# Optimization experiments

Measured on AMD Instinct MI355X. Metric: run time of the kernel, lower is better.

## Reference

```python
import jax, jax.numpy as jnp
import numpy as np

D_MODEL = 1024
N_HEAD = 16
B, S = 4, 1024


def setup_inputs() -> dict:
    key = jax.random.key(0)
    ks = jax.random.split(key, 10)
    f = lambda k, shp: jax.random.normal(k, shp, dtype=jnp.float32)
    return {
        "x": f(ks[0], (B, S, D_MODEL)),
        "y": f(ks[1], (B, S, D_MODEL)),
        "z": f(ks[2], (B, S, D_MODEL)),
        "mask": f(ks[3], (1, 1, S, S)) * 0.1,
        "wq_w": f(ks[4], (D_MODEL, D_MODEL)) * (D_MODEL ** -0.5),
        "wq_b": f(ks[5], (D_MODEL,)) * 0.02,
        "wk_w": f(ks[6], (D_MODEL, D_MODEL)) * (D_MODEL ** -0.5),
        "wk_b": f(ks[7], (D_MODEL,)) * 0.02,
        "wv_w": f(ks[8], (D_MODEL, D_MODEL)) * (D_MODEL ** -0.5),
        "wv_b": f(ks[9], (D_MODEL,)) * 0.02,
    }


def reference(x, y, z, mask, wq_w, wq_b, wk_w, wk_b, wv_w, wv_b):
    b, xl, d = x.shape
    hd = d // N_HEAD
    # linear projections (torch Linear: x @ W^T + b)
    q = x @ wq_w.T + wq_b
    k = y @ wk_w.T + wk_b
    v = z @ wv_w.T + wv_b
    # [B, H, L, hd]
    q = q.reshape(b, xl, N_HEAD, hd).transpose(0, 2, 1, 3)
    k = k.reshape(b, y.shape[1], N_HEAD, hd).transpose(0, 2, 1, 3)
    v = v.reshape(b, z.shape[1], N_HEAD, hd).transpose(0, 2, 1, 3)
    # NOTE: source scales by sqrt(d_model), not sqrt(head_dim)
    scale = 1.0 / jnp.sqrt(jnp.asarray(d, dtype=x.dtype))
    logits = jnp.einsum("bhqd,bhkd->bhqk", q, k) * scale
    score = jax.nn.softmax(logits, axis=-1)
    # mask added AFTER softmax (faithful to source)
    score = score + mask
    out = jnp.einsum("bhqk,bhkd->bhqd", score, v)
    return out.transpose(0, 2, 1, 3).reshape(b, xl, d)
```

## Files before the change

kernel.cpp:

```cpp
#include <hip/hip_runtime.h>
#include <hip/hip_bf16.h>
#include <cstdint>

typedef __bf16 bf16_t;
typedef __bf16 bf16x8 __attribute__((ext_vector_type(8)));
typedef __bf16 bf16x4 __attribute__((ext_vector_type(4)));
typedef float floatx4 __attribute__((ext_vector_type(4)));

typedef __attribute__((address_space(3))) uint32_t lds_u32_t;
typedef const __attribute__((address_space(1))) uint32_t g_u32_t;

#define MFMA_BF16(a, b, c) __builtin_amdgcn_mfma_f32_16x16x32_bf16((a), (b), (c), 0, 0, 0)

static constexpr int S = 1024;
static constexpr int HD = 64;

struct ConvArgs {
  const float* src[7];
  bf16_t* dst[7];
  int n[7];
};

__global__ __launch_bounds__(256) void convert_kernel(ConvArgs a) {
  const int j = blockIdx.y;
  const float4* __restrict__ s = (const float4*)a.src[j];
  bf16x4* __restrict__ d = (bf16x4*)a.dst[j];
  const int n4 = a.n[j] >> 2;
  for (int i = blockIdx.x * blockDim.x + threadIdx.x; i < n4; i += gridDim.x * blockDim.x) {
    float4 v = s[i];
    bf16x4 o;
    o[0] = (bf16_t)v.x; o[1] = (bf16_t)v.y; o[2] = (bf16_t)v.z; o[3] = (bf16_t)v.w;
    d[i] = o;
  }
}

struct GemmCfg {
  const bf16_t* A;
  const bf16_t* Bm;
  void* out;
  const float* bias;
  int mode;
};

union GemmSmem {
  struct { bf16_t A[128 * 64]; bf16_t B[128 * 64]; } ab;
  bf16_t C[128 * 136];
};

__global__ __launch_bounds__(256, 3) void gemm_nt_kernel(GemmCfg c0, GemmCfg c1, GemmCfg c2, int K) {
  GemmCfg cfg = (blockIdx.y == 0) ? c0 : (blockIdx.y == 1 ? c1 : c2);
  __shared__ GemmSmem u;
  __shared__ float bias_s[128];
  const int tid = threadIdx.x;
  const int wave = tid >> 6;
  const int lane = tid & 63;
  const int g = lane >> 4;
  const int cl = lane & 15;
  const int mq = (wave & 1) * 64;
  const int nq = (wave >> 1) * 64;

  const int xcd = blockIdx.x & 7, idx = blockIdx.x >> 3;
  int mb, nb;
  if (cfg.mode == 0) { mb = xcd * 4 + (idx & 3); nb = idx >> 2; }
  else               { nb = xcd * 4 + (idx & 3); mb = idx >> 2; }
  const int m0 = mb * 128, n0 = nb * 128;

  if (tid < 128) bias_s[tid] = cfg.bias[(cfg.mode == 0 ? n0 : m0) + tid];

  const int srow = tid >> 3;
  const int sch = (tid & 7) ^ (srow & 7);
  const bf16_t* Ag = cfg.A + (size_t)(m0 + srow) * K + sch * 8;
  const bf16_t* Bg = cfg.Bm + (size_t)(n0 + srow) * K + sch * 8;
  const int swz = cl & 7;

  floatx4 acc[4][4];
#pragma unroll
  for (int i = 0; i < 4; ++i)
#pragma unroll
    for (int j = 0; j < 4; ++j) acc[i][j] = floatx4{0.f, 0.f, 0.f, 0.f};

  const int kiters = K >> 6;
  for (int kt = 0; kt < kiters; ++kt) {
    __syncthreads();
#pragma unroll
    for (int i = 0; i < 4; ++i) {
      __builtin_amdgcn_global_load_lds((g_u32_t*)(const void*)(Ag + (size_t)(i * 32) * K),
                                       (lds_u32_t*)(void*)&u.ab.A[(i * 256 + tid) * 8], 16, 0, 0);
      __builtin_amdgcn_global_load_lds((g_u32_t*)(const void*)(Bg + (size_t)(i * 32) * K),
                                       (lds_u32_t*)(void*)&u.ab.B[(i * 256 + tid) * 8], 16, 0, 0);
    }
    Ag += 64;
    Bg += 64;
    __syncthreads();

#pragma unroll
    for (int kc = 0; kc < 2; ++kc) {
      bf16x8 af[4], bfr[4];
#pragma unroll
      for (int i = 0; i < 4; ++i)
        af[i] = *(const bf16x8*)&u.ab.A[(mq + i * 16 + cl) * 64 + ((kc * 4 + g) ^ swz) * 8];
#pragma unroll
      for (int j = 0; j < 4; ++j)
        bfr[j] = *(const bf16x8*)&u.ab.B[(nq + j * 16 + cl) * 64 + ((kc * 4 + g) ^ swz) * 8];
#pragma unroll
      for (int i = 0; i < 4; ++i)
#pragma unroll
        for (int j = 0; j < 4; ++j) acc[i][j] = MFMA_BF16(af[i], bfr[j], acc[i][j]);
    }
  }

  __syncthreads();
#pragma unroll
  for (int i = 0; i < 4; ++i)
#pragma unroll
    for (int j = 0; j < 4; ++j)
#pragma unroll
      for (int r = 0; r < 4; ++r) {
        const int ml = mq + i * 16 + g * 4 + r;
        const int nl = nq + j * 16 + cl;
        float v = acc[i][j][r] + bias_s[cfg.mode == 0 ? nl : ml];
        u.C[ml * 136 + nl] = (bf16_t)v;
      }
  __syncthreads();
#pragma unroll
  for (int it = 0; it < 8; ++it) {
    const int ix = it * 256 + tid;
    const int ml = ix >> 4, nc = ix & 15;
    bf16x8 val = *(const bf16x8*)&u.C[ml * 136 + nc * 8];
    const int m = m0 + ml, n = n0 + nc * 8;
    size_t addr;
    if (cfg.mode == 0)
      addr = (size_t)((m >> 10) * 16 + (n >> 6)) * 65536 + (m & 1023) * 64 + (n & 63);
    else
      addr = (size_t)((n >> 10) * 16 + (m >> 6)) * 65536 + (m & 63) * 1024 + (n & 1023);
    *(bf16x8*)&((bf16_t*)cfg.out)[addr] = val;
  }
}

__global__ __launch_bounds__(256, 2) void attn_kernel(const bf16_t* __restrict__ Q,
                                                      const bf16_t* __restrict__ Kb,
                                                      const bf16_t* __restrict__ Vt,
                                                      const bf16_t* __restrict__ Mk,
                                                      float* __restrict__ out) {
  __shared__ bf16_t Ks[128 * 64];
  __shared__ bf16_t Vs[64 * 128];
  __shared__ bf16_t Pbuf[4][32 * 136];
  const int tid = threadIdx.x;
  const int wave = tid >> 6, lane = tid & 63;
  const int g = lane >> 4, cl = lane & 15;
  const int bh = blockIdx.x & 63, qt = blockIdx.x >> 6;
  const int q0w = qt * 128 + wave * 32;
  const bf16_t* Qp = Q + (size_t)bh * (S * HD);
  const bf16_t* Kp = Kb + (size_t)bh * (S * HD);
  const bf16_t* Vp = Vt + (size_t)bh * (S * HD);
  bf16_t* Pw = &Pbuf[wave][0];

  const int krow = tid >> 3, kch = (tid & 7) ^ (krow & 7);
  const int vrow = tid >> 4, vch = (tid & 15) ^ (vrow & 7);
  const int sw = cl & 7;

  bf16x8 qf[2][2];
#pragma unroll
  for (int nj = 0; nj < 2; ++nj)
#pragma unroll
    for (int kc = 0; kc < 2; ++kc)
      qf[nj][kc] = *(const bf16x8*)&Qp[(size_t)(q0w + nj * 16 + cl) * HD + kc * 32 + g * 8];

  floatx4 o[2][4], o2[2][4];
#pragma unroll
  for (int mi = 0; mi < 2; ++mi)
#pragma unroll
    for (int nj = 0; nj < 4; ++nj) {
      o[mi][nj] = floatx4{0.f, 0.f, 0.f, 0.f};
      o2[mi][nj] = floatx4{0.f, 0.f, 0.f, 0.f};
    }
  float dsq[2] = {0.f, 0.f};

  for (int kt = 0; kt < 8; ++kt) {
    const int k0 = kt * 128;
    __syncthreads();
#pragma unroll
    for (int i = 0; i < 4; ++i)
      __builtin_amdgcn_global_load_lds(
          (g_u32_t*)(const void*)&Kp[(size_t)(k0 + i * 32 + krow) * HD + kch * 8],
          (lds_u32_t*)(void*)&Ks[(i * 256 + tid) * 8], 16, 0, 0);
#pragma unroll
    for (int i = 0; i < 4; ++i)
      __builtin_amdgcn_global_load_lds(
          (g_u32_t*)(const void*)&Vp[(size_t)(i * 16 + vrow) * S + k0 + vch * 8],
          (lds_u32_t*)(void*)&Vs[(i * 256 + tid) * 8], 16, 0, 0);
    __syncthreads();

#pragma unroll
    for (int mi = 0; mi < 8; ++mi) {
      bf16x8 kf0 = *(const bf16x8*)&Ks[(mi * 16 + cl) * 64 + ((0 + g) ^ sw) * 8];
      bf16x8 kf1 = *(const bf16x8*)&Ks[(mi * 16 + cl) * 64 + ((4 + g) ^ sw) * 8];
      floatx4 s0 = floatx4{0.f, 0.f, 0.f, 0.f}, s1 = floatx4{0.f, 0.f, 0.f, 0.f};
      s0 = MFMA_BF16(kf0, qf[0][0], s0);
      s0 = MFMA_BF16(kf1, qf[0][1], s0);
      s1 = MFMA_BF16(kf0, qf[1][0], s1);
      s1 = MFMA_BF16(kf1, qf[1][1], s1);
      bf16x4 p0, p1;
#pragma unroll
      for (int r = 0; r < 4; ++r) {
        float e0 = __expf(s0[r] * 0.03125f);
        float e1 = __expf(s1[r] * 0.03125f);
        dsq[0] += e0;
        dsq[1] += e1;
        p0[r] = (bf16_t)e0;
        p1[r] = (bf16_t)e1;
      }
      *(bf16x4*)&Pw[(cl)*136 + mi * 16 + g * 4] = p0;
      *(bf16x4*)&Pw[(16 + cl) * 136 + mi * 16 + g * 4] = p1;
    }

#pragma unroll
    for (int kc = 0; kc < 4; ++kc) {
      bf16x8 pa0 = *(const bf16x8*)&Pw[cl * 136 + kc * 32 + g * 8];
      bf16x8 pa1 = *(const bf16x8*)&Pw[(16 + cl) * 136 + kc * 32 + g * 8];
      bf16x8 ma0 = *(const bf16x8*)&Mk[(size_t)(q0w + cl) * S + k0 + kc * 32 + g * 8];
      bf16x8 ma1 = *(const bf16x8*)&Mk[(size_t)(q0w + 16 + cl) * S + k0 + kc * 32 + g * 8];
#pragma unroll
      for (int nj = 0; nj < 4; ++nj) {
        bf16x8 vf = *(const bf16x8*)&Vs[(nj * 16 + cl) * 128 + ((kc * 4 + g) ^ sw) * 8];
        o[0][nj] = MFMA_BF16(pa0, vf, o[0][nj]);
        o[1][nj] = MFMA_BF16(pa1, vf, o[1][nj]);
        o2[0][nj] = MFMA_BF16(ma0, vf, o2[0][nj]);
        o2[1][nj] = MFMA_BF16(ma1, vf, o2[1][nj]);
      }
    }
  }

#pragma unroll
  for (int nj = 0; nj < 2; ++nj) {
    dsq[nj] += __shfl_xor(dsq[nj], 16, 64);
    dsq[nj] += __shfl_xor(dsq[nj], 32, 64);
  }

  const int b = bh >> 4, h = bh & 15;
#pragma unroll
  for (int mi = 0; mi < 2; ++mi) {
#pragma unroll
    for (int r = 0; r < 4; ++r) {
      float dv = __shfl(dsq[mi], g * 4 + r, 64);
      float dinv = 1.0f / dv;
      const int srow = q0w + mi * 16 + g * 4 + r;
#pragma unroll
      for (int nj = 0; nj < 4; ++nj) {
        const int hd = nj * 16 + cl;
        out[((size_t)b * S + srow) * 1024 + h * HD + hd] = o[mi][nj][r] * dinv + o2[mi][nj][r];
      }
    }
  }
}

extern "C" void kernel_launch(void* const* d_in, const int* in_sizes, int n_in,
                              void* d_out, int out_size, void* d_ws, size_t ws_size,
                              hipStream_t stream) {
  const float* x = (const float*)d_in[0];
  const float* y = (const float*)d_in[1];
  const float* z = (const float*)d_in[2];
  const float* mask = (const float*)d_in[3];
  const float* wq_w = (const float*)d_in[4];
  const float* wq_b = (const float*)d_in[5];
  const float* wk_w = (const float*)d_in[6];
  const float* wk_b = (const float*)d_in[7];
  const float* wv_w = (const float*)d_in[8];
  const float* wv_b = (const float*)d_in[9];

  uint8_t* ws = (uint8_t*)d_ws;
  const size_t MB = 1u << 20;
  bf16_t* Xb = (bf16_t*)(ws + 0 * MB);
  bf16_t* Yb = (bf16_t*)(ws + 8 * MB);
  bf16_t* Zb = (bf16_t*)(ws + 16 * MB);
  bf16_t* Wqb = (bf16_t*)(ws + 24 * MB);
  bf16_t* Wkb = (bf16_t*)(ws + 26 * MB);
  bf16_t* Wvb = (bf16_t*)(ws + 28 * MB);
  bf16_t* Mb = (bf16_t*)(ws + 30 * MB);
  bf16_t* Qb = (bf16_t*)(ws + 32 * MB);
  bf16_t* Kb = (bf16_t*)(ws + 40 * MB);
  bf16_t* Vtb = (bf16_t*)(ws + 48 * MB);

  ConvArgs ca;
  ca.src[0] = x;    ca.dst[0] = Xb;  ca.n[0] = 4 * 1024 * 1024;
  ca.src[1] = y;    ca.dst[1] = Yb;  ca.n[1] = 4 * 1024 * 1024;
  ca.src[2] = z;    ca.dst[2] = Zb;  ca.n[2] = 4 * 1024 * 1024;
  ca.src[3] = wq_w; ca.dst[3] = Wqb; ca.n[3] = 1024 * 1024;
  ca.src[4] = wk_w; ca.dst[4] = Wkb; ca.n[4] = 1024 * 1024;
  ca.src[5] = wv_w; ca.dst[5] = Wvb; ca.n[5] = 1024 * 1024;
  ca.src[6] = mask; ca.dst[6] = Mb;  ca.n[6] = 1024 * 1024;
  convert_kernel<<<dim3(512, 7), 256, 0, stream>>>(ca);

  GemmCfg cq{Xb, Wqb, (void*)Qb, wq_b, 0};
  GemmCfg ck{Yb, Wkb, (void*)Kb, wk_b, 0};
  GemmCfg cv{Wvb, Zb, (void*)Vtb, wv_b, 1};
  gemm_nt_kernel<<<dim3(256, 3), 256, 0, stream>>>(cq, ck, cv, 1024);

  attn_kernel<<<dim3(512), 256, 0, stream>>>(Qb, Kb, Vtb, Mb, (float*)d_out);
}
```

Measured before the change: 178.2 us.

## Fuse fp32-to-bf16 activation conversion into projection GEMM tile loads

Drops the separate conversion pass over the x, y, z activations. The GEMM now reads fp32 activations directly, converts them to bf16 in registers and writes them into the swizzled LDS tile, while weights still come through the async global-to-LDS path. This avoids writing and re-reading 24 MB of bf16 intermediates. The cost is synchronous register-staged loads in the GEMM main loop with no async overlap, plus twice the global bytes per activation tile. The softmax exponent also switches from __expf to exp2f with a folded log2e scale.

```diff
diff --git a/kernel.cpp b/kernel.cpp
--- a/kernel.cpp
+++ b/kernel.cpp
@@ -1,6 +1,7 @@
 #include <hip/hip_runtime.h>
 #include <hip/hip_bf16.h>
 #include <cstdint>
+#include <cmath>
 
 typedef __bf16 bf16_t;
 typedef __bf16 bf16x8 __attribute__((ext_vector_type(8)));
@@ -16,9 +17,9 @@
 static constexpr int HD = 64;
 
 struct ConvArgs {
-  const float* src[7];
-  bf16_t* dst[7];
-  int n[7];
+  const float* src[4];
+  bf16_t* dst[4];
+  int n[4];
 };
 
 __global__ __launch_bounds__(256) void convert_kernel(ConvArgs a) {
@@ -35,8 +36,8 @@
 }
 
 struct GemmCfg {
-  const bf16_t* A;
-  const bf16_t* Bm;
+  const float* X;
+  const bf16_t* W;
   void* out;
   const float* bias;
   int mode;
@@ -67,30 +68,51 @@
 
   if (tid < 128) bias_s[tid] = cfg.bias[(cfg.mode == 0 ? n0 : m0) + tid];
 
-  const int srow = tid >> 3;
-  const int sch = (tid & 7) ^ (srow & 7);
-  const bf16_t* Ag = cfg.A + (size_t)(m0 + srow) * K + sch * 8;
-  const bf16_t* Bg = cfg.Bm + (size_t)(n0 + srow) * K + sch * 8;
+  const int xrow0 = (cfg.mode == 0) ? m0 : n0;
+  const int wrow0 = (cfg.mode == 0) ? n0 : m0;
+  bf16_t* Xs = (cfg.mode == 0) ? u.ab.A : u.ab.B;
+  bf16_t* Ws = (cfg.mode == 0) ? u.ab.B : u.ab.A;
+
+  const int wsr = tid >> 3;
+  const int wsc = (tid & 7) ^ (wsr & 7);
+  const bf16_t* Wg = cfg.W + (size_t)(wrow0 + wsr) * K + wsc * 8;
+
+  const int xr = tid >> 4;
+  const int xc = tid & 15;
+  const int xch = ((xc >> 1) ^ (xr & 7));
+  const int xslot = xch * 8 + (xc & 1) * 4;
+  const float* Xg = cfg.X + (size_t)(xrow0 + xr) * K + xc * 4;
+
+  floatx4 acc[4][4];
+#pragma unroll
+  for (int i = 0; i < 4; ++i)
+#pragma unroll
+    for (int j = 0; j < 4; ++j) acc[i][j] = floatx4{0.f, 0.f, 0.f, 0.f};
+
   const int swz = cl & 7;
-
-  floatx4 acc[4][4];
-#pragma unroll
-  for (int i = 0; i < 4; ++i)
-#pragma unroll
-    for (int j = 0; j < 4; ++j) acc[i][j] = floatx4{0.f, 0.f, 0.f, 0.f};
-
   const int kiters = K >> 6;
   for (int kt = 0; kt < kiters; ++kt) {
     __syncthreads();
 #pragma unroll
-    for (int i = 0; i < 4; ++i) {
-      __builtin_amdgcn_global_load_lds((g_u32_t*)(const void*)(Ag + (size_t)(i * 32) * K),
-                                       (lds_u32_t*)(void*)&u.ab.A[(i * 256 + tid) * 8], 16, 0, 0);
-      __builtin_amdgcn_global_load_lds((g_u32_t*)(const void*)(Bg + (size_t)(i * 32) * K),
-                                       (lds_u32_t*)(void*)&u.ab.B[(i * 256 + tid) * 8], 16, 0, 0);
-    }
-    Ag += 64;
-    Bg += 64;
+    for (int i = 0; i < 4; ++i)
+      __builtin_amdgcn_global_load_lds((g_u32_t*)(const void*)(Wg + (size_t)(i * 32) * K),
+                                       (lds_u32_t*)(void*)&Ws[(i * 256 + tid) * 8], 16, 0, 0);
+#pragma unroll
+    for (int ph = 0; ph < 2; ++ph) {
+      float4 f[4];
+#pragma unroll
+      for (int p = 0; p < 4; ++p)
+        f[p] = *(const float4*)(Xg + (size_t)((ph * 4 + p) * 16) * K);
+#pragma unroll
+      for (int p = 0; p < 4; ++p) {
+        bf16x4 o;
+        o[0] = (bf16_t)f[p].x; o[1] = (bf16_t)f[p].y;
+        o[2] = (bf16_t)f[p].z; o[3] = (bf16_t)f[p].w;
+        *(bf16x4*)&Xs[((ph * 4 + p) * 16 + xr) * 64 + xslot] = o;
+      }
+    }
+    Wg += 64;
+    Xg += 64;
     __syncthreads();
 
 #pragma unroll
@@ -176,6 +198,8 @@
     }
   float dsq[2] = {0.f, 0.f};
 
+  const float kLog2eOver32 = 0.04508422002778011f;
+
   for (int kt = 0; kt < 8; ++kt) {
     const int k0 = kt * 128;
     __syncthreads();
@@ -203,8 +227,8 @@
       bf16x4 p0, p1;
 #pragma unroll
       for (int r = 0; r < 4; ++r) {
-        float e0 = __expf(s0[r] * 0.03125f);
-        float e1 = __expf(s1[r] * 0.03125f);
+        float e0 = exp2f(s0[r] * kLog2eOver32);
+        float e1 = exp2f(s1[r] * kLog2eOver32);
         dsq[0] += e0;
         dsq[1] += e1;
         p0[r] = (bf16_t)e0;
@@ -270,30 +294,24 @@
 
   uint8_t* ws = (uint8_t*)d_ws;
   const size_t MB = 1u << 20;
-  bf16_t* Xb = (bf16_t*)(ws + 0 * MB);
-  bf16_t* Yb = (bf16_t*)(ws + 8 * MB);
-  bf16_t* Zb = (bf16_t*)(ws + 16 * MB);
-  bf16_t* Wqb = (bf16_t*)(ws + 24 * MB);
-  bf16_t* Wkb = (bf16_t*)(ws + 26 * MB);
-  bf16_t* Wvb = (bf16_t*)(ws + 28 * MB);
-  bf16_t* Mb = (bf16_t*)(ws + 30 * MB);
-  bf16_t* Qb = (bf16_t*)(ws + 32 * MB);
-  bf16_t* Kb = (bf16_t*)(ws + 40 * MB);
-  bf16_t* Vtb = (bf16_t*)(ws + 48 * MB);
+  bf16_t* Wqb = (bf16_t*)(ws + 0 * MB);
+  bf16_t* Wkb = (bf16_t*)(ws + 2 * MB);
+  bf16_t* Wvb = (bf16_t*)(ws + 4 * MB);
+  bf16_t* Mb = (bf16_t*)(ws + 6 * MB);
+  bf16_t* Qb = (bf16_t*)(ws + 8 * MB);
+  bf16_t* Kb = (bf16_t*)(ws + 16 * MB);
+  bf16_t* Vtb = (bf16_t*)(ws + 24 * MB);
 
   ConvArgs ca;
-  ca.src[0] = x;    ca.dst[0] = Xb;  ca.n[0] = 4 * 1024 * 1024;
-  ca.src[1] = y;    ca.dst[1] = Yb;  ca.n[1] = 4 * 1024 * 1024;
-  ca.src[2] = z;    ca.dst[2] = Zb;  ca.n[2] = 4 * 1024 * 1024;
-  ca.src[3] = wq_w; ca.dst[3] = Wqb; ca.n[3] = 1024 * 1024;
-  ca.src[4] = wk_w; ca.dst[4] = Wkb; ca.n[4] = 1024 * 1024;
-  ca.src[5] = wv_w; ca.dst[5] = Wvb; ca.n[5] = 1024 * 1024;
-  ca.src[6] = mask; ca.dst[6] = Mb;  ca.n[6] = 1024 * 1024;
-  convert_kernel<<<dim3(512, 7), 256, 0, stream>>>(ca);
-
-  GemmCfg cq{Xb, Wqb, (void*)Qb, wq_b, 0};
-  GemmCfg ck{Yb, Wkb, (void*)Kb, wk_b, 0};
-  GemmCfg cv{Wvb, Zb, (void*)Vtb, wv_b, 1};
+  ca.src[0] = wq_w; ca.dst[0] = Wqb; ca.n[0] = 1024 * 1024;
+  ca.src[1] = wk_w; ca.dst[1] = Wkb; ca.n[1] = 1024 * 1024;
+  ca.src[2] = wv_w; ca.dst[2] = Wvb; ca.n[2] = 1024 * 1024;
+  ca.src[3] = mask; ca.dst[3] = Mb;  ca.n[3] = 1024 * 1024;
+  convert_kernel<<<dim3(256, 4), 256, 0, stream>>>(ca);
+
+  GemmCfg cq{x, Wqb, (void*)Qb, wq_b, 0};
+  GemmCfg ck{y, Wkb, (void*)Kb, wk_b, 0};
+  GemmCfg cv{z, Wvb, (void*)Vtb, wv_b, 1};
   gemm_nt_kernel<<<dim3(256, 3), 256, 0, stream>>>(cq, ck, cv, 1024);
 
   attn_kernel<<<dim3(512), 256, 0, stream>>>(Qb, Kb, Vtb, Mb, (float*)d_out);
```

Measured after the change: 193.5 us. 1.09x slower.

## Shrink attention tile to 16 rows per wave and prefetch mask fragments

Applied to the files above, without the earlier changes.

Each wave in the attention kernel now handles 16 query rows instead of 32, so the grid doubles to 1024 blocks and launch bounds allow 4 blocks per CU. The P staging buffer shrinks to a 16x32 swizzled tile that is reused per 32-key chunk, which interleaves the softmax and PV MFMAs. Mask fragments for the next key tile are loaded into registers ahead of time to hide global latency. In exchange, K/V tiles are loaded into LDS twice as often per query, and register pressure rises from the prefetch.

```diff
diff --git a/kernel.cpp b/kernel.cpp
--- a/kernel.cpp
+++ b/kernel.cpp
@@ -1,6 +1,7 @@
 #include <hip/hip_runtime.h>
 #include <hip/hip_bf16.h>
 #include <cstdint>
+#include <cmath>
 
 typedef __bf16 bf16_t;
 typedef __bf16 bf16x8 __attribute__((ext_vector_type(8)));
@@ -137,19 +138,19 @@
   }
 }
 
-__global__ __launch_bounds__(256, 2) void attn_kernel(const bf16_t* __restrict__ Q,
+__global__ __launch_bounds__(256, 4) void attn_kernel(const bf16_t* __restrict__ Q,
                                                       const bf16_t* __restrict__ Kb,
                                                       const bf16_t* __restrict__ Vt,
                                                       const bf16_t* __restrict__ Mk,
                                                       float* __restrict__ out) {
   __shared__ bf16_t Ks[128 * 64];
   __shared__ bf16_t Vs[64 * 128];
-  __shared__ bf16_t Pbuf[4][32 * 136];
+  __shared__ bf16_t Pbuf[4][16 * 32];
   const int tid = threadIdx.x;
   const int wave = tid >> 6, lane = tid & 63;
   const int g = lane >> 4, cl = lane & 15;
   const int bh = blockIdx.x & 63, qt = blockIdx.x >> 6;
-  const int q0w = qt * 128 + wave * 32;
+  const int q0w = qt * 64 + wave * 16;
   const bf16_t* Qp = Q + (size_t)bh * (S * HD);
   const bf16_t* Kp = Kb + (size_t)bh * (S * HD);
   const bf16_t* Vp = Vt + (size_t)bh * (S * HD);
@@ -158,23 +159,25 @@
   const int krow = tid >> 3, kch = (tid & 7) ^ (krow & 7);
   const int vrow = tid >> 4, vch = (tid & 15) ^ (vrow & 7);
   const int sw = cl & 7;
-
-  bf16x8 qf[2][2];
-#pragma unroll
-  for (int nj = 0; nj < 2; ++nj)
-#pragma unroll
-    for (int kc = 0; kc < 2; ++kc)
-      qf[nj][kc] = *(const bf16x8*)&Qp[(size_t)(q0w + nj * 16 + cl) * HD + kc * 32 + g * 8];
-
-  floatx4 o[2][4], o2[2][4];
-#pragma unroll
-  for (int mi = 0; mi < 2; ++mi)
-#pragma unroll
-    for (int nj = 0; nj < 4; ++nj) {
-      o[mi][nj] = floatx4{0.f, 0.f, 0.f, 0.f};
-      o2[mi][nj] = floatx4{0.f, 0.f, 0.f, 0.f};
-    }
-  float dsq[2] = {0.f, 0.f};
+  const int pswz = (cl >> 2) & 3;
+
+  bf16x8 qf[2];
+#pragma unroll
+  for (int kc = 0; kc < 2; ++kc)
+    qf[kc] = *(const bf16x8*)&Qp[(size_t)(q0w + cl) * HD + kc * 32 + g * 8];
+
+  const bf16_t* Mr = Mk + (size_t)(q0w + cl) * S;
+  bf16x8 mf[4];
+#pragma unroll
+  for (int kc = 0; kc < 4; ++kc) mf[kc] = *(const bf16x8*)&Mr[kc * 32 + g * 8];
+
+  floatx4 o[4], o2[4];
+#pragma unroll
+  for (int nj = 0; nj < 4; ++nj) {
+    o[nj] = floatx4{0.f, 0.f, 0.f, 0.f};
+    o2[nj] = floatx4{0.f, 0.f, 0.f, 0.f};
+  }
+  float dsq = 0.f;
 
   for (int kt = 0; kt < 8; ++kt) {
     const int k0 = kt * 128;
@@ -189,67 +192,58 @@
       __builtin_amdgcn_global_load_lds(
           (g_u32_t*)(const void*)&Vp[(size_t)(i * 16 + vrow) * S + k0 + vch * 8],
           (lds_u32_t*)(void*)&Vs[(i * 256 + tid) * 8], 16, 0, 0);
-    __syncthreads();
-
-#pragma unroll
-    for (int mi = 0; mi < 8; ++mi) {
-      bf16x8 kf0 = *(const bf16x8*)&Ks[(mi * 16 + cl) * 64 + ((0 + g) ^ sw) * 8];
-      bf16x8 kf1 = *(const bf16x8*)&Ks[(mi * 16 + cl) * 64 + ((4 + g) ^ sw) * 8];
-      floatx4 s0 = floatx4{0.f, 0.f, 0.f, 0.f}, s1 = floatx4{0.f, 0.f, 0.f, 0.f};
-      s0 = MFMA_BF16(kf0, qf[0][0], s0);
-      s0 = MFMA_BF16(kf1, qf[0][1], s0);
-      s1 = MFMA_BF16(kf0, qf[1][0], s1);
-      s1 = MFMA_BF16(kf1, qf[1][1], s1);
-      bf16x4 p0, p1;
-#pragma unroll
-      for (int r = 0; r < 4; ++r) {
-        float e0 = __expf(s0[r] * 0.03125f);
-        float e1 = __expf(s1[r] * 0.03125f);
-        dsq[0] += e0;
-        dsq[1] += e1;
-        p0[r] = (bf16_t)e0;
-        p1[r] = (bf16_t)e1;
+
+    const int kn = (kt < 7) ? (k0 + 128) : 0;
+    bf16x8 mfn[4];
+#pragma unroll
+    for (int kc = 0; kc < 4; ++kc) mfn[kc] = *(const bf16x8*)&Mr[kn + kc * 32 + g * 8];
+    __syncthreads();
+
+#pragma unroll
+    for (int t = 0; t < 4; ++t) {
+#pragma unroll
+      for (int a = 0; a < 2; ++a) {
+        const int mi = t * 2 + a;
+        bf16x8 kf0 = *(const bf16x8*)&Ks[(mi * 16 + cl) * 64 + ((0 + g) ^ sw) * 8];
+        bf16x8 kf1 = *(const bf16x8*)&Ks[(mi * 16 + cl) * 64 + ((4 + g) ^ sw) * 8];
+        floatx4 s0 = floatx4{0.f, 0.f, 0.f, 0.f};
+        s0 = MFMA_BF16(kf0, qf[0], s0);
+        s0 = MFMA_BF16(kf1, qf[1], s0);
+        bf16x4 p0;
+#pragma unroll
+        for (int r = 0; r < 4; ++r) {
+          float e = __expf(s0[r] * 0.03125f);
+          dsq += e;
+          p0[r] = (bf16_t)e;
+        }
+        *(bf16x4*)&Pw[cl * 32 + (((a * 2 + (g >> 1)) ^ pswz) * 8) + (g & 1) * 4] = p0;
       }
-      *(bf16x4*)&Pw[(cl)*136 + mi * 16 + g * 4] = p0;
-      *(bf16x4*)&Pw[(16 + cl) * 136 + mi * 16 + g * 4] = p1;
-    }
-
-#pragma unroll
-    for (int kc = 0; kc < 4; ++kc) {
-      bf16x8 pa0 = *(const bf16x8*)&Pw[cl * 136 + kc * 32 + g * 8];
-      bf16x8 pa1 = *(const bf16x8*)&Pw[(16 + cl) * 136 + kc * 32 + g * 8];
-      bf16x8 ma0 = *(const bf16x8*)&Mk[(size_t)(q0w + cl) * S + k0 + kc * 32 + g * 8];
-      bf16x8 ma1 = *(const bf16x8*)&Mk[(size_t)(q0w + 16 + cl) * S + k0 + kc * 32 + g * 8];
+      bf16x8 pa = *(const bf16x8*)&Pw[cl * 32 + ((g ^ pswz) * 8)];
 #pragma unroll
       for (int nj = 0; nj < 4; ++nj) {
-        bf16x8 vf = *(const bf16x8*)&Vs[(nj * 16 + cl) * 128 + ((kc * 4 + g) ^ sw) * 8];
-        o[0][nj] = MFMA_BF16(pa0, vf, o[0][nj]);
-        o[1][nj] = MFMA_BF16(pa1, vf, o[1][nj]);
-        o2[0][nj] = MFMA_BF16(ma0, vf, o2[0][nj]);
-        o2[1][nj] = MFMA_BF16(ma1, vf, o2[1][nj]);
+        bf16x8 vf = *(const bf16x8*)&Vs[(nj * 16 + cl) * 128 + ((t * 4 + g) ^ sw) * 8];
+        o[nj] = MFMA_BF16(pa, vf, o[nj]);
+        o2[nj] = MFMA_BF16(mf[t], vf, o2[nj]);
       }
     }
-  }
-
-#pragma unroll
-  for (int nj = 0; nj < 2; ++nj) {
-    dsq[nj] += __shfl_xor(dsq[nj], 16, 64);
-    dsq[nj] += __shfl_xor(dsq[nj], 32, 64);
-  }
+
+#pragma unroll
+    for (int kc = 0; kc < 4; ++kc) mf[kc] = mfn[kc];
+  }
+
+  dsq += __shfl_xor(dsq, 16, 64);
+  dsq += __shfl_xor(dsq, 32, 64);
 
   const int b = bh >> 4, h = bh & 15;
 #pragma unroll
-  for (int mi = 0; mi < 2; ++mi) {
-#pragma unroll
-    for (int r = 0; r < 4; ++r) {
-      float dv = __shfl(dsq[mi], g * 4 + r, 64);
-      float dinv = 1.0f / dv;
-      const int srow = q0w + mi * 16 + g * 4 + r;
-#pragma unroll
-      for (int nj = 0; nj < 4; ++nj) {
-        const int hd = nj * 16 + cl;
-        out[((size_t)b * S + srow) * 1024 + h * HD + hd] = o[mi][nj][r] * dinv + o2[mi][nj][r];
-      }
+  for (int r = 0; r < 4; ++r) {
+    float dv = __shfl(dsq, g * 4 + r, 64);
+    float dinv = 1.0f / dv;
+    const int srow = q0w + g * 4 + r;
+#pragma unroll
+    for (int nj = 0; nj < 4; ++nj) {
+      const int hd = nj * 16 + cl;
+      out[((size_t)b * S + srow) * 1024 + h * HD + hd] = o[nj][r] * dinv + o2[nj][r];
     }
   }
 }
@@ -296,5 +290,5 @@
   GemmCfg cv{Wvb, Zb, (void*)Vtb, wv_b, 1};
   gemm_nt_kernel<<<dim3(256, 3), 256, 0, stream>>>(cq, ck, cv, 1024);
 
-  attn_kernel<<<dim3(512), 256, 0, stream>>>(Qb, Kb, Vtb, Mb, (float*)d_out);
-}
+  attn_kernel<<<dim3(1024), 256, 0, stream>>>(Qb, Kb, Vtb, Mb, (float*)d_out);
+}
```

Result: slower. 185.7 us (+4.2%).
